# Performance work log

Measured on AMD Instinct MI355X. Metric: run time of the kernel, lower is better.

Reference implementation:

```python
import jax, jax.numpy as jnp
import numpy as np

B, C, T = 512, 256, 256
E, K, G = 8, 5, 8
EPS = 1e-5


def setup_inputs() -> dict:
    key = jax.random.key(0)
    k1, k2, k3, k4 = jax.random.split(key, 4)
    x = jax.random.normal(k1, (B, C, T), dtype=jnp.float32)
    use_expert_i = jax.random.randint(k2, (B,), 0, E, dtype=jnp.int32)
    # per-expert Conv1d params: weight [E, Cout, Cin, K], bias [E, Cout]
    W = jax.random.normal(k3, (E, C, C, K), dtype=jnp.float32) * 0.05
    b = jax.random.normal(k4, (E, C), dtype=jnp.float32) * 0.05
    # per-expert GroupNorm affine params (torch default init: gamma=1, beta=0)
    gamma = jnp.ones((E, C), dtype=jnp.float32)
    beta = jnp.zeros((E, C), dtype=jnp.float32)
    return {"x": x, "use_expert_i": use_expert_i, "W": W, "b": b,
            "gamma": gamma, "beta": beta}


def _mish(y):
    return y * jnp.tanh(jax.nn.softplus(y))


def reference(x, use_expert_i, W, b, gamma, beta):
    # Top-1 one-hot routing => weight is exactly 1 for the selected expert, so
    # output[b] = Mish(GroupNorm(Conv1d_{e_b}(x[b]))). Gather per-sample params
    # instead of looping over experts (same math, vectorized).
    pad = K // 2
    Wb = W[use_expert_i]        # [B, Cout, Cin, K]
    bb = b[use_expert_i]        # [B, Cout]
    gb = gamma[use_expert_i]    # [B, Cout]
    betab = beta[use_expert_i]  # [B, Cout]

    def per_sample_conv(xi, wi, bi):
        # xi: [Cin, T], wi: [Cout, Cin, K] -> [Cout, T] ('same' padding)
        y = jax.lax.conv_general_dilated(xi[None], wi, window_strides=(1,),
                                         padding=[(pad, pad)])[0]
        return y + bi[:, None]

    y = jax.vmap(per_sample_conv)(x, Wb, bb)  # [B, C, T]

    # GroupNorm: normalize over (channels-in-group, length) per sample
    yg = y.reshape(B, G, C // G, T)
    mu = jnp.mean(yg, axis=(2, 3), keepdims=True)
    var = jnp.var(yg, axis=(2, 3), keepdims=True)
    yn = ((yg - mu) * jax.lax.rsqrt(var + EPS)).reshape(B, C, T)
    yn = yn * gb[:, :, None] + betab[:, :, None]
    return _mish(yn)
```

## Files before the change

kernel.cpp:

```cpp
#include <hip/hip_runtime.h>
#include <cmath>

constexpr int Bn = 512, Cn = 256, Tn = 256, En = 8;
constexpr float EPSf = 1e-5f;

using bf16x8 = __attribute__((ext_vector_type(8))) short;
using f32x4  = __attribute__((ext_vector_type(4))) float;

__device__ __forceinline__ ushort f2bf(float f) {
    uint u = __builtin_bit_cast(uint, f);
    uint r = u + 0x7FFFu + ((u >> 16) & 1u);
    return (ushort)(r >> 16);
}

__global__ __launch_bounds__(256)
void wconv_kernel(const float* __restrict__ Wf, ushort* __restrict__ Wws) {
    int idx = blockIdx.x * 256 + threadIdx.x;
    const float* src = Wf + (size_t)idx * 5;
    int ci = idx & 255, co = (idx >> 8) & 255, e = idx >> 16;
#pragma unroll
    for (int k = 0; k < 5; ++k)
        Wws[(((size_t)(e * 5 + k) * 256 + co) << 8) + ci] = f2bf(src[k]);
}

__global__ __launch_bounds__(256)
void xpose_kernel(const float* __restrict__ x, ushort* __restrict__ xT) {
    const int id = blockIdx.x;
    const int b  = id >> 5;
    const int cc = (id >> 3) & 3, tc = id & 7;
    const int ci0 = cc * 64, t0 = tc * 32;
    const int tid = threadIdx.x;

    __shared__ float ls[64][33];

    const int tl = tid & 31;
#pragma unroll
    for (int jj = 0; jj < 8; ++jj) {
        const int cil = (tid >> 5) * 8 + jj;
        ls[cil][tl] = x[((size_t)(b * 256 + ci0 + cil)) * 256 + t0 + tl];
    }
    __syncthreads();

    const int ciw = tid & 63;
#pragma unroll
    for (int jj = 0; jj < 8; ++jj) {
        const int tw = (tid >> 6) * 8 + jj;
        xT[((size_t)(b * 256 + t0 + tw)) * 256 + ci0 + ciw] = f2bf(ls[ciw][tw]);
    }
}

template<int MODE>
__global__ __launch_bounds__(256, 3)
void conv_gn_mish(const float* __restrict__ x, const ushort* __restrict__ xTw,
                  const int* __restrict__ expert,
                  const float* __restrict__ Wf, const ushort* __restrict__ Wws,
                  const float* __restrict__ bias, const float* __restrict__ gamma,
                  const float* __restrict__ beta, float* __restrict__ out)
{
    const int id = blockIdx.x;
    const int wg = (id & 7) * 256 + (id >> 3);
    const int b  = wg >> 2;
    const int gp = wg & 3;
    const int cb = gp * 64;
    const int e  = __builtin_amdgcn_readfirstlane(expert[b]);

    const int tid = threadIdx.x;
    const int w = tid >> 6, l = tid & 63, q = l >> 4, r = l & 15;
    const int tw = w * 64;

    __shared__ ushort xw[4][2][68 * 40];
    __shared__ float red[4][4];

    f32x4 acc[4][4];
#pragma unroll
    for (int m = 0; m < 4; ++m)
#pragma unroll
        for (int n = 0; n < 4; ++n) acc[m][n] = f32x4{0.f, 0.f, 0.f, 0.f};

    const int srow = l >> 2;
    const int slot = l & 3;
    const bf16x8 zv = {0, 0, 0, 0, 0, 0, 0, 0};
    bf16x8 g[5];

#define STAGE_LOAD(CI0) {                                                    \
        _Pragma("unroll")                                                    \
        for (int j = 0; j < 5; ++j) {                                        \
            const int row = j * 16 + srow;                                   \
            const int t = tw - 2 + row;                                      \
            const bool ok = (row < 68) && (t >= 0) && (t < Tn);              \
            if (MODE == 2) {                                                 \
                g[j] = ok ? *reinterpret_cast<const bf16x8*>(                \
                    xTw + ((size_t)(b * 256 + t)) * 256 + (CI0) + slot * 8)  \
                          : zv;                                              \
            } else {                                                         \
                bf16x8 a = zv;                                               \
                if (ok) {                                                    \
                    const float* xp = x + ((size_t)b * Cn + (CI0) + slot * 8) * Tn + t; \
                    _Pragma("unroll")                                        \
                    for (int jj = 0; jj < 8; ++jj)                           \
                        a[jj] = (short)f2bf(xp[jj * Tn]);                    \
                }                                                            \
                g[j] = a;                                                    \
            }                                                                \
        }                                                                    \
    }
#define STAGE_WRITE(BUF) {                                                   \
        ushort* dst = &xw[w][BUF][0];                                        \
        _Pragma("unroll")                                                    \
        for (int j = 0; j < 5; ++j) {                                        \
            const int row = j * 16 + srow;                                   \
            if (row < 68)                                                    \
                *reinterpret_cast<bf16x8*>(dst + row * 40 + slot * 8) = g[j];\
        }                                                                    \
    }

    STAGE_LOAD(0);
    STAGE_WRITE(0);
    STAGE_LOAD(32);

#pragma unroll 1
    for (int ct = 0; ct < 8; ++ct) {
        if (ct < 7) {
            STAGE_WRITE((ct + 1) & 1);
            if (ct < 6) STAGE_LOAD((ct + 2) * 32);
        }
        const int ci0 = ct * 32;
        const ushort* src = &xw[w][ct & 1][0];

#pragma unroll
        for (int k = 0; k < 5; ++k) {
            bf16x8 A[4];
#pragma unroll
            for (int m = 0; m < 4; ++m) {
                if (MODE >= 1) {
                    A[m] = *reinterpret_cast<const bf16x8*>(
                        Wws + (((size_t)((e * 5 + k) * 256 + cb + m * 16 + r)) << 8)
                            + ci0 + q * 8);
                } else {
                    bf16x8 a;
#pragma unroll
                    for (int j = 0; j < 8; ++j)
                        a[j] = (short)f2bf(
                            Wf[((size_t)(e * 256 + cb + m * 16 + r) * 256
                                + ci0 + q * 8 + j) * 5 + k]);
                    A[m] = a;
                }
            }
#pragma unroll
            for (int n = 0; n < 4; ++n) {
                const bf16x8 Bf = *reinterpret_cast<const bf16x8*>(
                    &src[(n * 16 + r + k) * 40 + q * 8]);
#pragma unroll
                for (int m = 0; m < 4; ++m)
                    acc[m][n] = __builtin_amdgcn_mfma_f32_16x16x32_bf16(
                        A[m], Bf, acc[m][n], 0, 0, 0);
            }
        }
    }
#undef STAGE_LOAD
#undef STAGE_WRITE

    float s1a = 0.f, s2a = 0.f, s1b = 0.f, s2b = 0.f;
#pragma unroll
    for (int m = 0; m < 4; ++m) {
#pragma unroll
        for (int i = 0; i < 4; ++i) {
            const float bv = bias[e * Cn + cb + m * 16 + q * 4 + i];
#pragma unroll
            for (int n = 0; n < 4; ++n) {
                const float val = acc[m][n][i] + bv;
                acc[m][n][i] = val;
                if (m < 2) { s1a += val; s2a += val * val; }
                else       { s1b += val; s2b += val * val; }
            }
        }
    }
#pragma unroll
    for (int off = 32; off; off >>= 1) {
        s1a += __shfl_xor(s1a, off); s2a += __shfl_xor(s2a, off);
        s1b += __shfl_xor(s1b, off); s2b += __shfl_xor(s2b, off);
    }
    if (l == 0) { red[w][0] = s1a; red[w][1] = s2a; red[w][2] = s1b; red[w][3] = s2b; }
    __syncthreads();
    const float S1a = red[0][0] + red[1][0] + red[2][0] + red[3][0];
    const float S2a = red[0][1] + red[1][1] + red[2][1] + red[3][1];
    const float S1b = red[0][2] + red[1][2] + red[2][2] + red[3][2];
    const float S2b = red[0][3] + red[1][3] + red[2][3] + red[3][3];

    constexpr float invn = 1.0f / (32 * 256);
    const float mua = S1a * invn, mub = S1b * invn;
    const float rsa = rsqrtf(fmaf(-mua, mua, S2a * invn) + EPSf);
    const float rsb = rsqrtf(fmaf(-mub, mub, S2b * invn) + EPSf);

#pragma unroll
    for (int m = 0; m < 4; ++m) {
        const float mu = (m < 2) ? mua : mub;
        const float rs = (m < 2) ? rsa : rsb;
#pragma unroll
        for (int i = 0; i < 4; ++i) {
            const int co = cb + m * 16 + q * 4 + i;
            const float sc = gamma[e * Cn + co] * rs;
            const float sh = beta[e * Cn + co] - mu * sc;
            float* orow = out + ((size_t)(b * Cn + co)) * Tn + tw + r;
#pragma unroll
            for (int n = 0; n < 4; ++n) {
                const float y = fmaf(acc[m][n][i], sc, sh);
                const float u  = __expf(y);
                const float t2 = u * (u + 2.f);
                const float ms = (y > 20.f) ? y : y * t2 / (t2 + 2.f);
                orow[n * 16] = ms;
            }
        }
    }
}

extern "C" void kernel_launch(void* const* d_in, const int* in_sizes, int n_in,
                              void* d_out, int out_size, void* d_ws, size_t ws_size,
                              hipStream_t stream) {
    const float* x      = (const float*)d_in[0];
    const int*   expert = (const int*)  d_in[1];
    const float* Wf     = (const float*)d_in[2];
    const float* bias   = (const float*)d_in[3];
    const float* gamma  = (const float*)d_in[4];
    const float* beta   = (const float*)d_in[5];
    float* out = (float*)d_out;

    const size_t WWS_BYTES = (size_t)En * 5 * 256 * 256 * 2;
    const size_t XT_BYTES  = (size_t)Bn * 256 * 256 * 2;

    ushort* Wws = (ushort*)d_ws;
    ushort* xTw = (ushort*)((char*)d_ws + WWS_BYTES);

    if (ws_size >= WWS_BYTES + XT_BYTES) {
        hipLaunchKernelGGL(wconv_kernel, dim3(2048), dim3(256), 0, stream, Wf, Wws);
        hipLaunchKernelGGL(xpose_kernel, dim3(16384), dim3(256), 0, stream, x, xTw);
        hipLaunchKernelGGL((conv_gn_mish<2>), dim3(2048), dim3(256), 0, stream,
                           x, xTw, expert, Wf, Wws, bias, gamma, beta, out);
    } else if (ws_size >= WWS_BYTES) {
        hipLaunchKernelGGL(wconv_kernel, dim3(2048), dim3(256), 0, stream, Wf, Wws);
        hipLaunchKernelGGL((conv_gn_mish<1>), dim3(2048), dim3(256), 0, stream,
                           x, nullptr, expert, Wf, Wws, bias, gamma, beta, out);
    } else {
        hipLaunchKernelGGL((conv_gn_mish<0>), dim3(2048), dim3(256), 0, stream,
                           x, nullptr, expert, Wf, nullptr, bias, gamma, beta, out);
    }
}
```

Before: 225.3 us.

## Read transposed bf16 activations directly from global memory, skipping LDS staging

Adds a conv_direct kernel for the path with full workspace. It loads MFMA B fragments for each kernel tap straight from the transposed bf16 x buffer in global memory, relying on L1/L2 for the overlapping taps, and drops the double-buffered LDS staging and its barriers. This removes LDS writes and syncs, but raises global/L1 traffic roughly fivefold for x and may expose load latency with no software pipelining.

```diff
diff --git a/kernel.cpp b/kernel.cpp
--- a/kernel.cpp
+++ b/kernel.cpp
@@ -49,13 +49,11 @@
     }
 }
 
-template<int MODE>
 __global__ __launch_bounds__(256, 3)
-void conv_gn_mish(const float* __restrict__ x, const ushort* __restrict__ xTw,
-                  const int* __restrict__ expert,
-                  const float* __restrict__ Wf, const ushort* __restrict__ Wws,
-                  const float* __restrict__ bias, const float* __restrict__ gamma,
-                  const float* __restrict__ beta, float* __restrict__ out)
+void conv_direct(const ushort* __restrict__ xTw, const int* __restrict__ expert,
+                 const ushort* __restrict__ Wws,
+                 const float* __restrict__ bias, const float* __restrict__ gamma,
+                 const float* __restrict__ beta, float* __restrict__ out)
 {
     const int id = blockIdx.x;
     const int wg = (id & 7) * 256 + (id >> 3);
@@ -68,6 +66,124 @@
     const int w = tid >> 6, l = tid & 63, q = l >> 4, r = l & 15;
     const int tw = w * 64;
 
+    __shared__ float red[4][4];
+
+    f32x4 acc[4][4];
+#pragma unroll
+    for (int m = 0; m < 4; ++m)
+#pragma unroll
+        for (int n = 0; n < 4; ++n) acc[m][n] = f32x4{0.f, 0.f, 0.f, 0.f};
+
+    const bf16x8 zv = {0, 0, 0, 0, 0, 0, 0, 0};
+    const ushort* xrow = xTw + ((size_t)b << 16) + q * 8;
+
+#pragma unroll 1
+    for (int ct = 0; ct < 8; ++ct) {
+        const int ci0 = ct * 32;
+
+#pragma unroll
+        for (int k = 0; k < 5; ++k) {
+            bf16x8 A[4];
+#pragma unroll
+            for (int m = 0; m < 4; ++m)
+                A[m] = *reinterpret_cast<const bf16x8*>(
+                    Wws + (((size_t)((e * 5 + k) * 256 + cb + m * 16 + r)) << 8)
+                        + ci0 + q * 8);
+
+#pragma unroll
+            for (int n = 0; n < 4; ++n) {
+                const int t = tw + n * 16 + r + k - 2;
+                bf16x8 Bf;
+                if ((w == 0 && n == 0) || (w == 3 && n == 3)) {
+                    const bool ok = ((unsigned)t) < 256u;
+                    const int tc = ok ? t : 2;
+                    Bf = *reinterpret_cast<const bf16x8*>(
+                        xrow + ((size_t)tc << 8) + ci0);
+                    if (!ok) Bf = zv;
+                } else {
+                    Bf = *reinterpret_cast<const bf16x8*>(
+                        xrow + ((size_t)t << 8) + ci0);
+                }
+#pragma unroll
+                for (int m = 0; m < 4; ++m)
+                    acc[m][n] = __builtin_amdgcn_mfma_f32_16x16x32_bf16(
+                        A[m], Bf, acc[m][n], 0, 0, 0);
+            }
+        }
+    }
+
+    float s1a = 0.f, s2a = 0.f, s1b = 0.f, s2b = 0.f;
+#pragma unroll
+    for (int m = 0; m < 4; ++m) {
+#pragma unroll
+        for (int i = 0; i < 4; ++i) {
+            const float bv = bias[e * Cn + cb + m * 16 + q * 4 + i];
+#pragma unroll
+            for (int n = 0; n < 4; ++n) {
+                const float val = acc[m][n][i] + bv;
+                acc[m][n][i] = val;
+                if (m < 2) { s1a += val; s2a += val * val; }
+                else       { s1b += val; s2b += val * val; }
+            }
+        }
+    }
+#pragma unroll
+    for (int off = 32; off; off >>= 1) {
+        s1a += __shfl_xor(s1a, off); s2a += __shfl_xor(s2a, off);
+        s1b += __shfl_xor(s1b, off); s2b += __shfl_xor(s2b, off);
+    }
+    if (l == 0) { red[w][0] = s1a; red[w][1] = s2a; red[w][2] = s1b; red[w][3] = s2b; }
+    __syncthreads();
+    const float S1a = red[0][0] + red[1][0] + red[2][0] + red[3][0];
+    const float S2a = red[0][1] + red[1][1] + red[2][1] + red[3][1];
+    const float S1b = red[0][2] + red[1][2] + red[2][2] + red[3][2];
+    const float S2b = red[0][3] + red[1][3] + red[2][3] + red[3][3];
+
+    constexpr float invn = 1.0f / (32 * 256);
+    const float mua = S1a * invn, mub = S1b * invn;
+    const float rsa = rsqrtf(fmaf(-mua, mua, S2a * invn) + EPSf);
+    const float rsb = rsqrtf(fmaf(-mub, mub, S2b * invn) + EPSf);
+
+#pragma unroll
+    for (int m = 0; m < 4; ++m) {
+        const float mu = (m < 2) ? mua : mub;
+        const float rs = (m < 2) ? rsa : rsb;
+#pragma unroll
+        for (int i = 0; i < 4; ++i) {
+            const int co = cb + m * 16 + q * 4 + i;
+            const float sc = gamma[e * Cn + co] * rs;
+            const float sh = beta[e * Cn + co] - mu * sc;
+            float* orow = out + ((size_t)(b * Cn + co)) * Tn + tw + r;
+#pragma unroll
+            for (int n = 0; n < 4; ++n) {
+                const float y = fmaf(acc[m][n][i], sc, sh);
+                const float u  = __expf(y);
+                const float t2 = u * (u + 2.f);
+                const float ms = (y > 20.f) ? y : y * t2 / (t2 + 2.f);
+                orow[n * 16] = ms;
+            }
+        }
+    }
+}
+
+template<int MODE>
+__global__ __launch_bounds__(256, 3)
+void conv_gn_mish_lds(const float* __restrict__ x, const int* __restrict__ expert,
+                      const float* __restrict__ Wf, const ushort* __restrict__ Wws,
+                      const float* __restrict__ bias, const float* __restrict__ gamma,
+                      const float* __restrict__ beta, float* __restrict__ out)
+{
+    const int id = blockIdx.x;
+    const int wg = (id & 7) * 256 + (id >> 3);
+    const int b  = wg >> 2;
+    const int gp = wg & 3;
+    const int cb = gp * 64;
+    const int e  = __builtin_amdgcn_readfirstlane(expert[b]);
+
+    const int tid = threadIdx.x;
+    const int w = tid >> 6, l = tid & 63, q = l >> 4, r = l & 15;
+    const int tw = w * 64;
+
     __shared__ ushort xw[4][2][68 * 40];
     __shared__ float red[4][4];
 
@@ -88,20 +204,14 @@
             const int row = j * 16 + srow;                                   \
             const int t = tw - 2 + row;                                      \
             const bool ok = (row < 68) && (t >= 0) && (t < Tn);              \
-            if (MODE == 2) {                                                 \
-                g[j] = ok ? *reinterpret_cast<const bf16x8*>(                \
-                    xTw + ((size_t)(b * 256 + t)) * 256 + (CI0) + slot * 8)  \
-                          : zv;                                              \
-            } else {                                                         \
-                bf16x8 a = zv;                                               \
-                if (ok) {                                                    \
-                    const float* xp = x + ((size_t)b * Cn + (CI0) + slot * 8) * Tn + t; \
-                    _Pragma("unroll")                                        \
-                    for (int jj = 0; jj < 8; ++jj)                           \
-                        a[jj] = (short)f2bf(xp[jj * Tn]);                    \
-                }                                                            \
-                g[j] = a;                                                    \
+            bf16x8 a = zv;                                                   \
+            if (ok) {                                                        \
+                const float* xp = x + ((size_t)b * Cn + (CI0) + slot * 8) * Tn + t; \
+                _Pragma("unroll")                                            \
+                for (int jj = 0; jj < 8; ++jj)                               \
+                    a[jj] = (short)f2bf(xp[jj * Tn]);                        \
             }                                                                \
+            g[j] = a;                                                        \
         }                                                                    \
     }
 #define STAGE_WRITE(BUF) {                                                   \
@@ -234,14 +344,14 @@
     if (ws_size >= WWS_BYTES + XT_BYTES) {
         hipLaunchKernelGGL(wconv_kernel, dim3(2048), dim3(256), 0, stream, Wf, Wws);
         hipLaunchKernelGGL(xpose_kernel, dim3(16384), dim3(256), 0, stream, x, xTw);
-        hipLaunchKernelGGL((conv_gn_mish<2>), dim3(2048), dim3(256), 0, stream,
-                           x, xTw, expert, Wf, Wws, bias, gamma, beta, out);
+        hipLaunchKernelGGL(conv_direct, dim3(2048), dim3(256), 0, stream,
+                           xTw, expert, Wws, bias, gamma, beta, out);
     } else if (ws_size >= WWS_BYTES) {
         hipLaunchKernelGGL(wconv_kernel, dim3(2048), dim3(256), 0, stream, Wf, Wws);
-        hipLaunchKernelGGL((conv_gn_mish<1>), dim3(2048), dim3(256), 0, stream,
-                           x, nullptr, expert, Wf, Wws, bias, gamma, beta, out);
+        hipLaunchKernelGGL((conv_gn_mish_lds<1>), dim3(2048), dim3(256), 0, stream,
+                           x, expert, Wf, Wws, bias, gamma, beta, out);
     } else {
-        hipLaunchKernelGGL((conv_gn_mish<0>), dim3(2048), dim3(256), 0, stream,
-                           x, nullptr, expert, Wf, nullptr, bias, gamma, beta, out);
-    }
-}
+        hipLaunchKernelGGL((conv_gn_mish_lds<0>), dim3(2048), dim3(256), 0, stream,
+                           x, expert, Wf, nullptr, bias, gamma, beta, out);
+    }
+}
```

After: 464.2 us. 2.06x slower.
